# Performance work log

Measured on AMD Instinct MI355X. Metric: run time of the kernel, lower is better.

Reference implementation:

```python
import jax, jax.numpy as jnp
import numpy as np

B, S, D, F, E, K = 4, 2048, 1024, 4096, 8, 2


def setup_inputs() -> dict:
    key = jax.random.key(0)
    ks = jax.random.split(key, 8)
    x = jax.random.normal(ks[0], (B, S, D), dtype=jnp.float32)
    # torch nn.Linear stores W as (out, in); stack per-expert params on leading E axis
    router_w = jax.random.normal(ks[1], (E, D), dtype=jnp.float32) * 0.02
    w1_w = jax.random.normal(ks[2], (E, F, D), dtype=jnp.float32) * 0.02
    w1_b = jax.random.normal(ks[3], (E, F), dtype=jnp.float32) * 0.02
    w2_w = jax.random.normal(ks[4], (E, D, F), dtype=jnp.float32) * 0.02
    w2_b = jax.random.normal(ks[5], (E, D), dtype=jnp.float32) * 0.02
    wg_w = jax.random.normal(ks[6], (E, F, D), dtype=jnp.float32) * 0.02
    wg_b = jax.random.normal(ks[7], (E, F), dtype=jnp.float32) * 0.02
    return {"x": x, "router_w": router_w, "w1_w": w1_w, "w1_b": w1_b,
            "w2_w": w2_w, "w2_b": w2_b, "wg_w": wg_w, "wg_b": wg_b}


def reference(x, router_w, w1_w, w1_b, w2_w, w2_b, wg_w, wg_b):
    # router: softmax then top-k (identical to torch.topk(softmax(...)))
    probs = jax.nn.softmax(jnp.einsum('bsd,ed->bse', x, router_w), axis=-1)
    token_probs, probs_idx = jax.lax.top_k(probs, K)  # (b,s,k)
    # combine the k gate weights into a dense (b,s,E) gate (top-k indices are distinct,
    # so summing one-hot slots reproduces the original scatter + sum over k exactly)
    gates = jnp.sum(token_probs[..., None] *
                    jax.nn.one_hot(probs_idx, E, dtype=x.dtype), axis=-2)  # (b,s,E)
    gates_e = jnp.moveaxis(gates, -1, 0)  # (E,b,s)

    def body(acc, params):
        w1w, w1b, w2w, w2b, wgw, wgb, g = params
        y = jax.nn.gelu(jnp.einsum('bsd,fd->bsf', x, wgw) + wgb, approximate=False)
        h = y * (jnp.einsum('bsd,fd->bsf', x, w1w) + w1b)
        out = jnp.einsum('bsf,df->bsd', h, w2w) + w2b
        return acc + out * g[..., None], None

    acc0 = jnp.zeros_like(x)
    out, _ = jax.lax.scan(body, acc0, (w1_w, w1_b, w2_w, w2_b, wg_w, wg_b, gates_e))
    return out
```

## Files before the change

kernel.cpp:

```cpp
#include <hip/hip_runtime.h>
#include <hip/hip_bf16.h>

#define TOK 8192
#define DD 1024
#define FF 4096
#define EE 8
#define NPAIR 16384

typedef __attribute__((ext_vector_type(8))) short short8;
typedef __attribute__((ext_vector_type(4))) short short4v;
typedef __attribute__((ext_vector_type(4))) float f32x4;

#define VMCNT8()  asm volatile("s_waitcnt vmcnt(8)" ::: "memory")
#define VMCNT0()  asm volatile("s_waitcnt vmcnt(0)" ::: "memory")
#define LGKM0()   asm volatile("s_waitcnt lgkmcnt(0)" ::: "memory")
#define BARRIER() asm volatile("s_barrier" ::: "memory")

__device__ __forceinline__ void async16(const void* g, void* l) {
  __builtin_amdgcn_global_load_lds((const __attribute__((address_space(1))) void*)g,
                                   (__attribute__((address_space(3))) void*)l, 16, 0, 0);
}

__device__ __forceinline__ short bfc(float f) {
  return __builtin_bit_cast(short, (__bf16)f);
}
__device__ __forceinline__ short8 cvt8(f32x4 a, f32x4 b) {
  short8 r;
  r[0]=bfc(a[0]); r[1]=bfc(a[1]); r[2]=bfc(a[2]); r[3]=bfc(a[3]);
  r[4]=bfc(b[0]); r[5]=bfc(b[1]); r[6]=bfc(b[2]); r[7]=bfc(b[3]);
  return r;
}
__device__ __forceinline__ int swz4(int r) { return (r ^ (r >> 2)) & 3; }

__global__ __launch_bounds__(256) void cvt_bf16_kernel(const float* __restrict__ src,
                                                       short* __restrict__ dst, int n8) {
  int i = blockIdx.x * 256 + threadIdx.x;
  const int stride = gridDim.x * 256;
  for (; i < n8; i += stride) {
    f32x4 a = ((const f32x4*)src)[2*i];
    f32x4 b = ((const f32x4*)src)[2*i + 1];
    ((short8*)dst)[i] = cvt8(a, b);
  }
}

__global__ __launch_bounds__(256) void cvt_interleave(const float* __restrict__ wgw,
    const float* __restrict__ w1w, short* __restrict__ wB) {
  const int b = blockIdx.x;
  const int e = b >> 12;
  const int f = b & 4095;
  const int g = f >> 4, j = f & 15;
  const int tid = threadIdx.x;
  const int u = tid & 127;
  const float* src = ((tid < 128) ? wgw : w1w) + (size_t)b * DD;
  const size_t drow = (size_t)e * (2*FF) + 32*g + j + ((tid < 128) ? 0 : 16);
  f32x4 a = ((const f32x4*)src)[2*u];
  f32x4 c = ((const f32x4*)src)[2*u + 1];
  ((short8*)(wB + drow * DD))[u] = cvt8(a, c);
}

__global__ __launch_bounds__(64) void router_kernel(const float* __restrict__ x,
    const float* __restrict__ rw, int* __restrict__ counts, int* __restrict__ lists,
    float* __restrict__ gates, int* __restrict__ eids, short* __restrict__ xb, int write_xb) {
  const int t = blockIdx.x;
  const int l = threadIdx.x;
  const f32x4* xr = (const f32x4*)(x + (size_t)t * DD);
  f32x4 xv[4];
#pragma unroll
  for (int i = 0; i < 4; i++) xv[i] = xr[l + 64 * i];
  if (write_xb) {
    short4v* xo = (short4v*)(xb + (size_t)t * DD);
#pragma unroll
    for (int i = 0; i < 4; i++) {
      short4v o; o[0]=bfc(xv[i][0]); o[1]=bfc(xv[i][1]); o[2]=bfc(xv[i][2]); o[3]=bfc(xv[i][3]);
      xo[l + 64 * i] = o;
    }
  }
  float lg[EE];
#pragma unroll
  for (int e = 0; e < EE; e++) {
    const f32x4* wr = (const f32x4*)(rw + e * DD);
    float s = 0.f;
#pragma unroll
    for (int i = 0; i < 4; i++) {
      f32x4 w = wr[l + 64 * i];
      s += xv[i][0]*w[0] + xv[i][1]*w[1] + xv[i][2]*w[2] + xv[i][3]*w[3];
    }
#pragma unroll
    for (int off = 32; off > 0; off >>= 1) s += __shfl_down(s, off, 64);
    lg[e] = s;
  }
  if (l == 0) {
    float mx = lg[0];
#pragma unroll
    for (int e = 1; e < EE; e++) mx = fmaxf(mx, lg[e]);
    float p[EE]; float den = 0.f;
#pragma unroll
    for (int e = 0; e < EE; e++) { p[e] = expf(lg[e] - mx); den += p[e]; }
    int i1 = 0;
#pragma unroll
    for (int e = 1; e < EE; e++) if (p[e] > p[i1]) i1 = e;
    int i2 = (i1 == 0) ? 1 : 0;
#pragma unroll
    for (int e = 0; e < EE; e++) if (e != i1 && p[e] > p[i2]) i2 = e;
    float inv = 1.f / den;
    gates[t*2+0] = p[i1] * inv;  eids[t*2+0] = i1;
    gates[t*2+1] = p[i2] * inv;  eids[t*2+1] = i2;
    int p1 = atomicAdd(&counts[i1], 1); lists[i1*TOK + p1] = t*2 + 0;
    int p2 = atomicAdd(&counts[i2], 1); lists[i2*TOK + p2] = t*2 + 1;
  }
}

#define TBUF 16384

#define STGA(buf, t) do { const int ko=(t)*32; short* dd=&ldsm[(buf)*TBUF]; \
    async16(aS1+ko, dd + wid*512); async16(aS2+ko, dd + 4096 + wid*512); } while(0)
#define STGB(buf, t) do { const int ko=(t)*32; short* dd=&ldsm[(buf)*TBUF + 8192]; \
    async16(bS1+ko, dd + wid*512); async16(bS2+ko, dd + 4096 + wid*512); } while(0)
#define RDA(buf, mi) (*(const short8*)&ldsm[(buf)*TBUF + (wr*128+(mi)*16+ln15)*32 + ((g ^ swz4(wr*128+(mi)*16+ln15))*8)])
#define RDB(buf, ni) (*(const short8*)&ldsm[(buf)*TBUF + 8192 + (wc*64+(ni)*16+ln15)*32 + ((g ^ swz4(wc*64+(ni)*16+ln15))*8)])

#define MFMA_BF16 __builtin_amdgcn_mfma_f32_16x16x32_bf16

#define KLOOP(NT)                                                              \
  STGA(0,0); STGB(0,0); STGA(1,1); STGB(1,1); STGA(2,2); STGB(2,2);            \
  VMCNT8(); BARRIER();                                                         \
  _Pragma("unroll 1")                                                          \
  for (int t = 0; t < (NT); t++) {                                             \
    const int cur = t & 3, pf = (t + 3) & 3;                                   \
    const int tp = (t + 3 < (NT)) ? t + 3 : 0;       \
    short8 a[8], b[4];                                                         \
    _Pragma("unroll")                                                          \
    for (int mi = 0; mi < 8; mi++) a[mi] = RDA(cur, mi);                       \
    _Pragma("unroll")                                                          \
    for (int ni = 0; ni < 4; ni++) b[ni] = RDB(cur, ni);                       \
    STGA(pf, tp); STGB(pf, tp);                                                \
    VMCNT8();                                                                  \
    LGKM0();                                                                   \
    BARRIER();                                                                 \
    __builtin_amdgcn_s_setprio(1);                                             \
    _Pragma("unroll")                                                          \
    for (int mi = 0; mi < 8; mi++) {                                           \
      _Pragma("unroll")                                                        \
      for (int ni = 0; ni < 4; ni++)                                           \
        acc[mi][ni] = MFMA_BF16(a[mi], b[ni], acc[mi][ni], 0, 0, 0);           \
    }                                                                          \
    __builtin_amdgcn_s_setprio(0);                                             \
  }                                                                            \
  VMCNT0();

__global__ __launch_bounds__(512, 1) void stage_a8(
    const short* __restrict__ xb, const short* __restrict__ wB,
    const float* __restrict__ wgb, const float* __restrict__ w1b,
    const int* __restrict__ counts, const int* __restrict__ lists,
    short* __restrict__ hbuf, int f0chunk, int Fc) {

  const int NBX = gridDim.x, NBY = gridDim.y;
  const int q = NBX * NBY;
  const int lin = blockIdx.x + NBX * (blockIdx.y + NBY * blockIdx.z);
  const int orig = (lin & 7) * q + (lin >> 3);
  const int e = orig / q;
  const int m = orig - e * q;
  const int by = m % NBY;
  const int bx = m / NBY;

  const int cnt = counts[e];
  const int row0 = bx * 256;
  if (row0 >= cnt) return;
  const int R0 = f0chunk * 2 + by * 256;

  __shared__ short ldsm[4 * TBUF];
  __shared__ int s_pair[256];

  const int tid = threadIdx.x;
  const int wid = tid >> 6;
  const int lane = tid & 63;
  const int ln15 = lane & 15, g = lane >> 4;
  const int wr = wid >> 2, wc = wid & 3;

  if (tid < 256) {
    int r = row0 + tid;
    s_pair[tid] = (r < cnt) ? lists[e*TOK + r] : 0;
  }
  __syncthreads();

  const int r1 = tid >> 2, s1 = tid & 3;
  const int r2 = r1 + 128;
  const int l1 = s1 ^ swz4(r1);
  const int l2 = s1 ^ swz4(r2);
  const short* aS1 = xb + (size_t)(s_pair[r1] >> 1) * DD + l1 * 8;
  const short* aS2 = xb + (size_t)(s_pair[r2] >> 1) * DD + l2 * 8;
  const short* bS1 = wB + ((size_t)e * (2*FF) + R0 + r1) * DD + l1 * 8;
  const short* bS2 = wB + ((size_t)e * (2*FF) + R0 + r2) * DD + l2 * 8;

  f32x4 acc[8][4] = {};

  KLOOP(32)

  const float* wgb_e = wgb + e * FF;
  const float* w1b_e = w1b + e * FF;
  float bgv[2], b1v[2]; int fl[2];
#pragma unroll
  for (int m2 = 0; m2 < 2; m2++) {
    int fg = (R0 + wc*64 + m2*32) / 2 + ln15;
    bgv[m2] = wgb_e[fg];
    b1v[m2] = w1b_e[fg];
    fl[m2] = fg - f0chunk;
  }
#pragma unroll
  for (int mi = 0; mi < 8; mi++) {
    int trb = wr*128 + mi*16 + (g << 2);
#pragma unroll
    for (int m2 = 0; m2 < 2; m2++) {
#pragma unroll
      for (int j = 0; j < 4; j++) {
        int tr = trb + j;
        if (row0 + tr < cnt) {
          int pair = s_pair[tr];
          float hg = acc[mi][2*m2][j] + bgv[m2];
          float h1 = acc[mi][2*m2+1][j] + b1v[m2];
          float gl = 0.5f * hg * (1.f + erff(hg * 0.70710678118f));
          hbuf[(size_t)pair * Fc + fl[m2]] = bfc(gl * h1);
        }
      }
    }
  }
}

__global__ __launch_bounds__(512, 1) void stage_b8(
    const short* __restrict__ hbuf, const short* __restrict__ w2wb,
    const int* __restrict__ counts, const int* __restrict__ lists,
    float* __restrict__ ybuf, int Fc) {

  const int NBX = gridDim.x, NBY = gridDim.y;
  const int q = NBX * NBY;
  const int lin = blockIdx.x + NBX * (blockIdx.y + NBY * blockIdx.z);
  const int orig = (lin & 7) * q + (lin >> 3);
  const int e = orig / q;
  const int m = orig - e * q;
  const int by = m % NBY;
  const int bx = m / NBY;

  const int cnt = counts[e];
  const int row0 = bx * 256;
  if (row0 >= cnt) return;
  const int d0 = by * 256;

  __shared__ short ldsm[4 * TBUF];
  __shared__ int s_pair[256];

  const int tid = threadIdx.x;
  const int wid = tid >> 6;
  const int lane = tid & 63;
  const int ln15 = lane & 15, g = lane >> 4;
  const int wr = wid >> 2, wc = wid & 3;

  if (tid < 256) {
    int r = row0 + tid;
    s_pair[tid] = (r < cnt) ? lists[e*TOK + r] : 0;
  }
  __syncthreads();

  const int r1 = tid >> 2, s1 = tid & 3;
  const int r2 = r1 + 128;
  const int l1 = s1 ^ swz4(r1);
  const int l2 = s1 ^ swz4(r2);
  const short* aS1 = hbuf + (size_t)s_pair[r1] * Fc + l1 * 8;
  const short* aS2 = hbuf + (size_t)s_pair[r2] * Fc + l2 * 8;
  const short* bS1 = w2wb + ((size_t)e * DD + d0 + r1) * FF + l1 * 8;
  const short* bS2 = w2wb + ((size_t)e * DD + d0 + r2) * FF + l2 * 8;

  f32x4 acc[8][4] = {};
  const int NT = Fc >> 5;

  KLOOP(NT)

#pragma unroll
  for (int mi = 0; mi < 8; mi++) {
    int trb = wr*128 + mi*16 + (g << 2);
#pragma unroll
    for (int j = 0; j < 4; j++) {
      int tr = trb + j;
      if (row0 + tr < cnt) {
        int pair = s_pair[tr];
        float* yrow = ybuf + (size_t)pair * DD;
#pragma unroll
        for (int ni = 0; ni < 4; ni++) {
          int d = d0 + wc*64 + ni*16 + ln15;
          yrow[d] = acc[mi][ni][j];
        }
      }
    }
  }
}

__global__ __launch_bounds__(256) void combine_kernel(const float* __restrict__ yb,
    const float* __restrict__ w2b, const float* __restrict__ gates,
    const int* __restrict__ eids, float* __restrict__ out) {
  const int t = blockIdx.x;
  const int tid = threadIdx.x;
  const float g0 = gates[2*t], g1 = gates[2*t+1];
  const int e0 = eids[2*t], e1 = eids[2*t+1];
  f32x4 y0 = ((const f32x4*)(yb + (size_t)(2*t) * DD))[tid];
  f32x4 y1 = ((const f32x4*)(yb + (size_t)(2*t+1) * DD))[tid];
  f32x4 c0 = ((const f32x4*)(w2b + (size_t)e0 * DD))[tid];
  f32x4 c1 = ((const f32x4*)(w2b + (size_t)e1 * DD))[tid];
  f32x4 o;
#pragma unroll
  for (int i = 0; i < 4; i++) o[i] = g0 * (y0[i] + c0[i]) + g1 * (y1[i] + c1[i]);
  ((f32x4*)(out + (size_t)t * DD))[tid] = o;
}

#define BB_LDS (128*64)
__global__ __launch_bounds__(256, 2) void stage_b_bf(
    const short* __restrict__ hbuf, const short* __restrict__ w2wb, const float* __restrict__ w2b,
    const int* __restrict__ counts, const int* __restrict__ lists, const float* __restrict__ gates,
    float* __restrict__ out, int f0chunk, int Fc, int addbias) {

  const int lin = blockIdx.x + 64 * (blockIdx.y + 8 * blockIdx.z);
  const int orig = (lin & 7) * 512 + (lin >> 3);
  const int bx = orig & 63;
  const int by = (orig >> 6) & 7;
  const int e  = orig >> 9;

  const int cnt = counts[e];
  const int row0 = bx * 128;
  if (row0 >= cnt) return;
  const int d0 = by * 128;

  __shared__ short lA[2 * BB_LDS];
  __shared__ short lB[2 * BB_LDS];
  __shared__ int s_pair[128];

  const int tid = threadIdx.x;
  const int wid = tid >> 6;
  const int lane = tid & 63;

  if (tid < 128) {
    int r = row0 + tid;
    s_pair[tid] = (r < cnt) ? lists[e*TOK + r] : 0;
  }
  __syncthreads();

  const short* aSrc[4]; const short* bSrc[4];
#pragma unroll
  for (int p = 0; p < 4; p++) {
    int j = p * 256 + tid;
    int r = j >> 3;
    int sl = (j & 7) ^ (r & 7);
    aSrc[p] = hbuf + (size_t)s_pair[r] * Fc + sl * 8;
    bSrc[p] = w2wb + ((size_t)e * DD + d0 + r) * FF + f0chunk + sl * 8;
  }

  f32x4 acc[4][4] = {};
  const int wr = wid >> 1, wc = wid & 1;
  const int NT = Fc >> 6;

#pragma unroll
  for (int p = 0; p < 4; p++) async16(aSrc[p], &lA[p*2048 + wid*512]);
#pragma unroll
  for (int p = 0; p < 4; p++) async16(bSrc[p], &lB[p*2048 + wid*512]);

  for (int t = 0; t < NT; t++) {
    const int cur = t & 1;
    if (t + 1 < NT) {
      const int nb = cur ^ 1;
      const int kf = (t + 1) * 64;
#pragma unroll
      for (int p = 0; p < 4; p++) async16(aSrc[p] + kf, &lA[nb*BB_LDS + p*2048 + wid*512]);
#pragma unroll
      for (int p = 0; p < 4; p++) async16(bSrc[p] + kf, &lB[nb*BB_LDS + p*2048 + wid*512]);
      VMCNT8();
    } else {
      VMCNT0();
    }
    BARRIER();

    const short* LA = lA + cur * BB_LDS;
    const short* LB = lB + cur * BB_LDS;
#pragma unroll
    for (int kk = 0; kk < 2; kk++) {
      short8 a[4], b[4];
#pragma unroll
      for (int mi = 0; mi < 4; mi++) {
        int r = wr*64 + mi*16 + (lane & 15);
        int u = (kk*4 + (lane >> 4)) ^ (r & 7);
        a[mi] = *(const short8*)(LA + r*64 + u*8);
      }
#pragma unroll
      for (int ni = 0; ni < 4; ni++) {
        int r = wc*64 + ni*16 + (lane & 15);
        int u = (kk*4 + (lane >> 4)) ^ (r & 7);
        b[ni] = *(const short8*)(LB + r*64 + u*8);
      }
#pragma unroll
      for (int mi = 0; mi < 4; mi++)
#pragma unroll
        for (int ni = 0; ni < 4; ni++)
          acc[mi][ni] = MFMA_BF16(a[mi], b[ni], acc[mi][ni], 0, 0, 0);
    }
    BARRIER();
  }

  const float* w2b_e = w2b + e * DD;
#pragma unroll
  for (int mi = 0; mi < 4; mi++) {
    int trb = wr*64 + mi*16 + ((lane >> 4) << 2);
#pragma unroll
    for (int j = 0; j < 4; j++) {
      int tr = trb + j;
      if (row0 + tr < cnt) {
        int pair = s_pair[tr];
        int t = pair >> 1;
        float gt = gates[pair];
        float* orow = out + (size_t)t * DD;
#pragma unroll
        for (int ni = 0; ni < 4; ni++) {
          int d = d0 + wc*64 + ni*16 + (lane & 15);
          float v = acc[mi][ni][j] * gt;
          if (addbias) v += w2b_e[d] * gt;
          atomicAdd(orow + d, v);
        }
      }
    }
  }
}

__global__ __launch_bounds__(256, 2) void stage_a_f32(
    const float* __restrict__ x, const float* __restrict__ wgw, const float* __restrict__ wgb,
    const float* __restrict__ w1w, const float* __restrict__ w1b,
    const int* __restrict__ counts, const int* __restrict__ lists,
    short* __restrict__ hbuf, int f0chunk, int Fc) {

  const int e = blockIdx.z;
  const int cnt = counts[e];
  const int row0 = blockIdx.x * 128;
  if (row0 >= cnt) return;
  const int fc0 = blockIdx.y * 128;
  const int fg0 = f0chunk + fc0;

  __shared__ float lA[128 * 32];
  __shared__ float lBg[128 * 32];
  __shared__ float lB1[128 * 32];
  __shared__ int s_pair[128];

  const int tid = threadIdx.x;
  const int wid = tid >> 6;
  const int lane = tid & 63;

  if (tid < 128) {
    int r = row0 + tid;
    s_pair[tid] = (r < cnt) ? lists[e*TOK + r] : 0;
  }
  __syncthreads();

  const float* aSrc[4]; const float* gSrc[4]; const float* oSrc[4];
#pragma unroll
  for (int p = 0; p < 4; p++) {
    int j = p * 256 + tid;
    int r = j >> 3;
    int sl = (j & 7) ^ (r & 7);
    aSrc[p] = x + (size_t)(s_pair[r] >> 1) * DD + sl * 4;
    gSrc[p] = wgw + ((size_t)e * FF + fg0 + r) * DD + sl * 4;
    oSrc[p] = w1w + ((size_t)e * FF + fg0 + r) * DD + sl * 4;
  }

  f32x4 accg[4][4] = {}; f32x4 acc1[4][4] = {};
  const int wr = wid >> 1, wc = wid & 1;

  for (int k0 = 0; k0 < DD; k0 += 32) {
#pragma unroll
    for (int p = 0; p < 4; p++) async16(aSrc[p] + k0, &lA[p*1024 + wid*256]);
#pragma unroll
    for (int p = 0; p < 4; p++) async16(gSrc[p] + k0, &lBg[p*1024 + wid*256]);
#pragma unroll
    for (int p = 0; p < 4; p++) async16(oSrc[p] + k0, &lB1[p*1024 + wid*256]);
    __syncthreads();

    short8 a[4], bg[4], b1[4];
#pragma unroll
    for (int mi = 0; mi < 4; mi++) {
      int r = wr*64 + mi*16 + (lane & 15);
      int g2 = (lane >> 4) * 2;
      const f32x4* Ar = (const f32x4*)&lA[r * 32];
      a[mi] = cvt8(Ar[g2 ^ (r & 7)], Ar[(g2 + 1) ^ (r & 7)]);
    }
#pragma unroll
    for (int ni = 0; ni < 4; ni++) {
      int r = wc*64 + ni*16 + (lane & 15);
      int g2 = (lane >> 4) * 2;
      const f32x4* Bg = (const f32x4*)&lBg[r * 32];
      const f32x4* B1 = (const f32x4*)&lB1[r * 32];
      bg[ni] = cvt8(Bg[g2 ^ (r & 7)], Bg[(g2 + 1) ^ (r & 7)]);
      b1[ni] = cvt8(B1[g2 ^ (r & 7)], B1[(g2 + 1) ^ (r & 7)]);
    }
#pragma unroll
    for (int mi = 0; mi < 4; mi++)
#pragma unroll
      for (int ni = 0; ni < 4; ni++) {
        accg[mi][ni] = MFMA_BF16(a[mi], bg[ni], accg[mi][ni], 0, 0, 0);
        acc1[mi][ni] = MFMA_BF16(a[mi], b1[ni], acc1[mi][ni], 0, 0, 0);
      }
    __syncthreads();
  }

  const float* wgb_e = wgb + e * FF;
  const float* w1b_e = w1b + e * FF;
#pragma unroll
  for (int mi = 0; mi < 4; mi++) {
    int trb = wr*64 + mi*16 + ((lane >> 4) << 2);
#pragma unroll
    for (int ni = 0; ni < 4; ni++) {
      int c = wc*64 + ni*16 + (lane & 15);
      float bgv = wgb_e[fg0 + c];
      float b1v = w1b_e[fg0 + c];
#pragma unroll
      for (int j = 0; j < 4; j++) {
        int tr = trb + j;
        if (row0 + tr < cnt) {
          int pair = s_pair[tr];
          float hg = accg[mi][ni][j] + bgv;
          float h1 = acc1[mi][ni][j] + b1v;
          float gl = 0.5f * hg * (1.f + erff(hg * 0.70710678118f));
          hbuf[(size_t)pair * Fc + fc0 + c] = bfc(gl * h1);
        }
      }
    }
  }
}

__global__ __launch_bounds__(256, 2) void stage_b_f32(
    const short* __restrict__ hbuf, const float* __restrict__ w2w, const float* __restrict__ w2b,
    const int* __restrict__ counts, const int* __restrict__ lists, const float* __restrict__ gates,
    float* __restrict__ out, int f0chunk, int Fc, int addbias) {

  const int e = blockIdx.z;
  const int cnt = counts[e];
  const int row0 = blockIdx.x * 128;
  if (row0 >= cnt) return;
  const int d0 = blockIdx.y * 128;

  __shared__ short lA[128 * 64];
  __shared__ float lB[128 * 64];
  __shared__ int s_pair[128];

  const int tid = threadIdx.x;
  const int wid = tid >> 6;
  const int lane = tid & 63;

  if (tid < 128) {
    int r = row0 + tid;
    s_pair[tid] = (r < cnt) ? lists[e*TOK + r] : 0;
  }
  __syncthreads();

  const short* aSrc[4];
#pragma unroll
  for (int p = 0; p < 4; p++) {
    int j = p * 256 + tid;
    int r = j >> 3;
    int sl = (j & 7) ^ (r & 7);
    aSrc[p] = hbuf + (size_t)s_pair[r] * Fc + sl * 8;
  }
  const float* bSrc[8];
#pragma unroll
  for (int p = 0; p < 8; p++) {
    int j = p * 256 + tid;
    int r = j >> 4;
    int sl = (j & 15) ^ (r & 7);
    bSrc[p] = w2w + ((size_t)e * DD + d0 + r) * FF + f0chunk + sl * 4;
  }

  f32x4 acc[4][4] = {};
  const int wr = wid >> 1, wc = wid & 1;

  for (int kf = 0; kf < Fc; kf += 64) {
#pragma unroll
    for (int p = 0; p < 4; p++) async16(aSrc[p] + kf, &lA[p*2048 + wid*512]);
#pragma unroll
    for (int p = 0; p < 8; p++) async16(bSrc[p] + kf, &lB[p*1024 + wid*256]);
    __syncthreads();

#pragma unroll
    for (int kk = 0; kk < 2; kk++) {
      short8 a[4]; short8 b[4];
#pragma unroll
      for (int mi = 0; mi < 4; mi++) {
        int r = wr*64 + mi*16 + (lane & 15);
        int u = (kk*4 + (lane >> 4)) ^ (r & 7);
        a[mi] = ((const short8*)(lA + r * 64))[u];
      }
#pragma unroll
      for (int ni = 0; ni < 4; ni++) {
        int r = wc*64 + ni*16 + (lane & 15);
        int g2 = (kk*4 + (lane >> 4)) * 2;
        const f32x4* Br = (const f32x4*)(lB + r * 64);
        b[ni] = cvt8(Br[g2 ^ (r & 7)], Br[(g2 + 1) ^ (r & 7)]);
      }
#pragma unroll
      for (int mi = 0; mi < 4; mi++)
#pragma unroll
        for (int ni = 0; ni < 4; ni++)
          acc[mi][ni] = MFMA_BF16(a[mi], b[ni], acc[mi][ni], 0, 0, 0);
    }
    __syncthreads();
  }

  const float* w2b_e = w2b + e * DD;
#pragma unroll
  for (int mi = 0; mi < 4; mi++) {
    int trb = wr*64 + mi*16 + ((lane >> 4) << 2);
#pragma unroll
    for (int j = 0; j < 4; j++) {
      int tr = trb + j;
      if (row0 + tr < cnt) {
        int pair = s_pair[tr];
        int t = pair >> 1;
        float gt = gates[pair];
        float* orow = out + (size_t)t * DD;
#pragma unroll
        for (int ni = 0; ni < 4; ni++) {
          int d = d0 + wc*64 + ni*16 + (lane & 15);
          float v = acc[mi][ni][j] * gt;
          if (addbias) v += w2b_e[d] * gt;
          atomicAdd(orow + d, v);
        }
      }
    }
  }
}

extern "C" void kernel_launch(void* const* d_in, const int* in_sizes, int n_in,
                              void* d_out, int out_size, void* d_ws, size_t ws_size,
                              hipStream_t stream) {
  const float* x   = (const float*)d_in[0];
  const float* rw  = (const float*)d_in[1];
  const float* w1w = (const float*)d_in[2];
  const float* w1b = (const float*)d_in[3];
  const float* w2w = (const float*)d_in[4];
  const float* w2b = (const float*)d_in[5];
  const float* wgw = (const float*)d_in[6];
  const float* wgb = (const float*)d_in[7];
  float* out = (float*)d_out;

  char* ws = (char*)d_ws;
  size_t off = 0;
  int* counts = (int*)(ws + off); off += 128;
  int* lists  = (int*)(ws + off); off += (size_t)EE * TOK * 4;
  float* gates = (float*)(ws + off); off += (size_t)NPAIR * 4;
  int* eids = (int*)(ws + off); off += (size_t)NPAIR * 4;
  const size_t base0 = off;

  const size_t WELEM = (size_t)EE * FF * DD;
  const size_t bf_need = base0 + (size_t)TOK*DD*2 + 2*WELEM*2 + WELEM*2;

  hipMemsetAsync(counts, 0, 128, stream);

  const int cands[6] = {4096, 2048, 1024, 512, 256, 128};

  if (bf_need + (size_t)NPAIR * 128 * 2 <= ws_size) {
    off = base0;
    short* xb   = (short*)(ws + off); off += (size_t)TOK * DD * 2;
    short* wB   = (short*)(ws + off); off += 2 * WELEM * 2;
    short* w2wb = (short*)(ws + off); off += WELEM * 2;
    short* hbuf = (short*)(ws + off);
    float* ybuf = (float*)wB;

    int Fc = 128;
    for (int i = 0; i < 6; i++)
      if (off + (size_t)NPAIR * cands[i] * 2 <= ws_size) { Fc = cands[i]; break; }

    router_kernel<<<dim3(TOK), dim3(64), 0, stream>>>(x, rw, counts, lists, gates, eids, xb, 1);
    cvt_interleave<<<dim3(EE*FF), dim3(256), 0, stream>>>(wgw, w1w, wB);
    cvt_bf16_kernel<<<dim3(2048), dim3(256), 0, stream>>>(w2w, w2wb, (int)(WELEM/8));

    if (Fc == 4096) {
      stage_a8<<<dim3(32, (2*Fc)/256, EE), dim3(512), 0, stream>>>(
          xb, wB, wgb, w1b, counts, lists, hbuf, 0, Fc);
      stage_b8<<<dim3(32, DD/256, EE), dim3(512), 0, stream>>>(
          hbuf, w2wb, counts, lists, ybuf, Fc);
      combine_kernel<<<dim3(TOK), dim3(256), 0, stream>>>(ybuf, w2b, gates, eids, out);
    } else {
      hipMemsetAsync(out, 0, (size_t)TOK * DD * 4, stream);
      for (int f0 = 0; f0 < FF; f0 += Fc) {
        stage_a8<<<dim3(32, (2*Fc)/256, EE), dim3(512), 0, stream>>>(
            xb, wB, wgb, w1b, counts, lists, hbuf, f0, Fc);
        stage_b_bf<<<dim3(64, DD/128, EE), dim3(256), 0, stream>>>(
            hbuf, w2wb, w2b, counts, lists, gates, out, f0, Fc, f0 == 0);
      }
    }
  } else {
    short* hbuf = (short*)(ws + base0);
    int Fc = 128;
    for (int i = 0; i < 6; i++)
      if (base0 + (size_t)NPAIR * cands[i] * 2 <= ws_size) { Fc = cands[i]; break; }

    hipMemsetAsync(out, 0, (size_t)TOK * DD * 4, stream);
    router_kernel<<<dim3(TOK), dim3(64), 0, stream>>>(x, rw, counts, lists, gates, eids, nullptr, 0);

    for (int f0 = 0; f0 < FF; f0 += Fc) {
      dim3 ga(64, Fc / 128, EE);
      stage_a_f32<<<ga, dim3(256), 0, stream>>>(x, wgw, wgb, w1w, w1b, counts, lists, hbuf, f0, Fc);
      dim3 gb(64, DD / 128, EE);
      stage_b_f32<<<gb, dim3(256), 0, stream>>>(hbuf, w2w, w2b, counts, lists, gates, out, f0, Fc, f0 == 0);
    }
  }
}
```

Baseline: 1.009 ms.

## Double-buffer MFMA operand registers so LDS reads overlap the previous tile's MFMAs

```diff
diff --git a/kernel.cpp b/kernel.cpp
--- a/kernel.cpp
+++ b/kernel.cpp
@@ -15,6 +15,7 @@
 #define VMCNT0()  asm volatile("s_waitcnt vmcnt(0)" ::: "memory")
 #define LGKM0()   asm volatile("s_waitcnt lgkmcnt(0)" ::: "memory")
 #define BARRIER() asm volatile("s_barrier" ::: "memory")
+#define SCHEDB()  __builtin_amdgcn_sched_barrier(0)
 
 __device__ __forceinline__ void async16(const void* g, void* l) {
   __builtin_amdgcn_global_load_lds((const __attribute__((address_space(1))) void*)g,
@@ -121,30 +122,54 @@
 
 #define MFMA_BF16 __builtin_amdgcn_mfma_f32_16x16x32_bf16
 
-#define KLOOP(NT)                                                              \
-  STGA(0,0); STGB(0,0); STGA(1,1); STGB(1,1); STGA(2,2); STGB(2,2);            \
-  VMCNT8(); BARRIER();                                                         \
-  _Pragma("unroll 1")                                                          \
-  for (int t = 0; t < (NT); t++) {                                             \
-    const int cur = t & 3, pf = (t + 3) & 3;                                   \
-    const int tp = (t + 3 < (NT)) ? t + 3 : 0;       \
-    short8 a[8], b[4];                                                         \
-    _Pragma("unroll")                                                          \
-    for (int mi = 0; mi < 8; mi++) a[mi] = RDA(cur, mi);                       \
-    _Pragma("unroll")                                                          \
-    for (int ni = 0; ni < 4; ni++) b[ni] = RDB(cur, ni);                       \
+#define KBODY(tt, RC, RN, NT)                                                  \
+  {                                                                            \
+    const int pf = ((tt) + 3) & 3;                                             \
+    const int tp = ((tt) + 3 < (NT)) ? (tt) + 3 : 0;   \
     STGA(pf, tp); STGB(pf, tp);                                                \
+    SCHEDB();                                                                  \
     VMCNT8();                                                                  \
+    SCHEDB();                                                                  \
     LGKM0();                                                                   \
-    BARRIER();                                                                 \
+    SCHEDB();                                                                  \
+    __builtin_amdgcn_s_barrier();                                              \
+    SCHEDB();                                                                  \
+    if ((tt) + 1 < (NT)) {                                                     \
+      const int nb = ((tt) + 1) & 3;                                           \
+      _Pragma("unroll")                                                        \
+      for (int mi = 0; mi < 8; mi++) RN##a[mi] = RDA(nb, mi);                  \
+      _Pragma("unroll")                                                        \
+      for (int ni = 0; ni < 4; ni++) RN##b[ni] = RDB(nb, ni);                  \
+    }                                                                          \
+    SCHEDB();                                                                  \
     __builtin_amdgcn_s_setprio(1);                                             \
     _Pragma("unroll")                                                          \
-    for (int mi = 0; mi < 8; mi++) {                                           \
+    for (int mi = 0; mi < 8; mi++)                                             \
       _Pragma("unroll")                                                        \
       for (int ni = 0; ni < 4; ni++)                                           \
-        acc[mi][ni] = MFMA_BF16(a[mi], b[ni], acc[mi][ni], 0, 0, 0);           \
-    }                                                                          \
+        acc[mi][ni] = MFMA_BF16(RC##a[mi], RC##b[ni], acc[mi][ni], 0, 0, 0);   \
     __builtin_amdgcn_s_setprio(0);                                             \
+    SCHEDB();                                                                  \
+  }
+
+#define KLOOP2(NT)                                                             \
+  short8 Pa[8], Pb[4], Qa[8], Qb[4];                                           \
+  STGA(0,0); STGB(0,0); STGA(1,1); STGB(1,1); STGA(2,2); STGB(2,2);            \
+  SCHEDB();                                                                    \
+  VMCNT8();                                                                    \
+  SCHEDB();                                                                    \
+  __builtin_amdgcn_s_barrier();                                                \
+  SCHEDB();                                                                    \
+  _Pragma("unroll")                                                            \
+  for (int mi = 0; mi < 8; mi++) Pa[mi] = RDA(0, mi);                          \
+  _Pragma("unroll")                                                            \
+  for (int ni = 0; ni < 4; ni++) Pb[ni] = RDB(0, ni);                          \
+  SCHEDB();                                                                    \
+  _Pragma("unroll 1")                                                          \
+  for (int t2 = 0; t2 < (NT)/2; t2++) {                                        \
+    const int t0 = 2*t2;                                                       \
+    KBODY(t0,     P, Q, NT);                                                   \
+    KBODY(t0 + 1, Q, P, NT);                                                   \
   }                                                                            \
   VMCNT0();
 
@@ -194,7 +219,7 @@
 
   f32x4 acc[8][4] = {};
 
-  KLOOP(32)
+  KLOOP2(32)
 
   const float* wgb_e = wgb + e * FF;
   const float* w1b_e = w1b + e * FF;
@@ -272,7 +297,7 @@
   f32x4 acc[8][4] = {};
   const int NT = Fc >> 5;
 
-  KLOOP(NT)
+  KLOOP2(NT)
 
 #pragma unroll
   for (int mi = 0; mi < 8; mi++) {
```

Result: slower. 1.062 ms (+5.2%).

## Switch GEMM K-loop to double-buffered 64-wide K tiles with 8-way swizzle

Applied to the files above, without the earlier changes.

```diff
diff --git a/kernel.cpp b/kernel.cpp
--- a/kernel.cpp
+++ b/kernel.cpp
@@ -15,6 +15,7 @@
 #define VMCNT0()  asm volatile("s_waitcnt vmcnt(0)" ::: "memory")
 #define LGKM0()   asm volatile("s_waitcnt lgkmcnt(0)" ::: "memory")
 #define BARRIER() asm volatile("s_barrier" ::: "memory")
+#define SCHEDB()  __builtin_amdgcn_sched_barrier(0)
 
 __device__ __forceinline__ void async16(const void* g, void* l) {
   __builtin_amdgcn_global_load_lds((const __attribute__((address_space(1))) void*)g,
@@ -30,7 +31,6 @@
   r[4]=bfc(b[0]); r[5]=bfc(b[1]); r[6]=bfc(b[2]); r[7]=bfc(b[3]);
   return r;
 }
-__device__ __forceinline__ int swz4(int r) { return (r ^ (r >> 2)) & 3; }
 
 __global__ __launch_bounds__(256) void cvt_bf16_kernel(const float* __restrict__ src,
                                                        short* __restrict__ dst, int n8) {
@@ -110,41 +110,56 @@
   }
 }
 
-#define TBUF 16384
-
-#define STGA(buf, t) do { const int ko=(t)*32; short* dd=&ldsm[(buf)*TBUF]; \
-    async16(aS1+ko, dd + wid*512); async16(aS2+ko, dd + 4096 + wid*512); } while(0)
-#define STGB(buf, t) do { const int ko=(t)*32; short* dd=&ldsm[(buf)*TBUF + 8192]; \
-    async16(bS1+ko, dd + wid*512); async16(bS2+ko, dd + 4096 + wid*512); } while(0)
-#define RDA(buf, mi) (*(const short8*)&ldsm[(buf)*TBUF + (wr*128+(mi)*16+ln15)*32 + ((g ^ swz4(wr*128+(mi)*16+ln15))*8)])
-#define RDB(buf, ni) (*(const short8*)&ldsm[(buf)*TBUF + 8192 + (wc*64+(ni)*16+ln15)*32 + ((g ^ swz4(wc*64+(ni)*16+ln15))*8)])
+#define TB2 32768
+
+#define STG2(buf, t) do { const int ko=(t)*64;                                 \
+    _Pragma("unroll")                                                          \
+    for (int p = 0; p < 4; p++) {                                              \
+      async16(aS[p] + ko, &ldsm[(buf)*TB2 + p*4096 + wid*512]);                \
+      async16(bS[p] + ko, &ldsm[(buf)*TB2 + 16384 + p*4096 + wid*512]);        \
+    } } while(0)
+
+#define RD_A(buf, kk, mi) (*(const short8*)&ldsm[(buf)*TB2 + (wr*128+(mi)*16+ln15)*64 + ((((kk)*4+g) ^ ((wr*128+(mi)*16+ln15)&7))*8)])
+#define RD_B(buf, kk, ni) (*(const short8*)&ldsm[(buf)*TB2 + 16384 + (wc*64+(ni)*16+ln15)*64 + ((((kk)*4+g) ^ ((wc*64+(ni)*16+ln15)&7))*8)])
 
 #define MFMA_BF16 __builtin_amdgcn_mfma_f32_16x16x32_bf16
 
-#define KLOOP(NT)                                                              \
-  STGA(0,0); STGB(0,0); STGA(1,1); STGB(1,1); STGA(2,2); STGB(2,2);            \
-  VMCNT8(); BARRIER();                                                         \
+#define KLOOP3(NT)                                                             \
+  STG2(0, 0);                                                                  \
+  SCHEDB();                                                                    \
   _Pragma("unroll 1")                                                          \
   for (int t = 0; t < (NT); t++) {                                             \
-    const int cur = t & 3, pf = (t + 3) & 3;                                   \
-    const int tp = (t + 3 < (NT)) ? t + 3 : 0;       \
-    short8 a[8], b[4];                                                         \
+    const int cur = t & 1;                                                     \
+    if (t + 1 < (NT)) {                                                        \
+      STG2(cur ^ 1, t + 1);                                                    \
+      SCHEDB();                                                                \
+      VMCNT8();                                                                \
+    } else {                                                                   \
+      VMCNT0();                                                                \
+    }                                                                          \
+    SCHEDB();                                                                  \
+    __builtin_amdgcn_s_barrier();                                              \
+    SCHEDB();                                                                  \
     _Pragma("unroll")                                                          \
-    for (int mi = 0; mi < 8; mi++) a[mi] = RDA(cur, mi);                       \
-    _Pragma("unroll")                                                          \
-    for (int ni = 0; ni < 4; ni++) b[ni] = RDB(cur, ni);                       \
-    STGA(pf, tp); STGB(pf, tp);                                                \
-    VMCNT8();                                                                  \
+    for (int kk = 0; kk < 2; kk++) {                                           \
+      short8 a[8], b[4];                                                       \
+      _Pragma("unroll")                                                        \
+      for (int mi = 0; mi < 8; mi++) a[mi] = RD_A(cur, kk, mi);                \
+      _Pragma("unroll")                                                        \
+      for (int ni = 0; ni < 4; ni++) b[ni] = RD_B(cur, kk, ni);                \
+      __builtin_amdgcn_s_setprio(1);                                           \
+      _Pragma("unroll")                                                        \
+      for (int mi = 0; mi < 8; mi++)                                           \
+        _Pragma("unroll")                                                      \
+        for (int ni = 0; ni < 4; ni++)                                         \
+          acc[mi][ni] = MFMA_BF16(a[mi], b[ni], acc[mi][ni], 0, 0, 0);         \
+      __builtin_amdgcn_s_setprio(0);                                           \
+    }                                                                          \
+    SCHEDB();                                                                  \
     LGKM0();                                                                   \
-    BARRIER();                                                                 \
-    __builtin_amdgcn_s_setprio(1);                                             \
-    _Pragma("unroll")                                                          \
-    for (int mi = 0; mi < 8; mi++) {                                           \
-      _Pragma("unroll")                                                        \
-      for (int ni = 0; ni < 4; ni++)                                           \
-        acc[mi][ni] = MFMA_BF16(a[mi], b[ni], acc[mi][ni], 0, 0, 0);           \
-    }                                                                          \
-    __builtin_amdgcn_s_setprio(0);                                             \
+    SCHEDB();                                                                  \
+    __builtin_amdgcn_s_barrier();                                              \
+    SCHEDB();                                                                  \
   }                                                                            \
   VMCNT0();
 
@@ -168,7 +183,7 @@
   if (row0 >= cnt) return;
   const int R0 = f0chunk * 2 + by * 256;
 
-  __shared__ short ldsm[4 * TBUF];
+  __shared__ short ldsm[2 * TB2];
   __shared__ int s_pair[256];
 
   const int tid = threadIdx.x;
@@ -183,18 +198,19 @@
   }
   __syncthreads();
 
-  const int r1 = tid >> 2, s1 = tid & 3;
-  const int r2 = r1 + 128;
-  const int l1 = s1 ^ swz4(r1);
-  const int l2 = s1 ^ swz4(r2);
-  const short* aS1 = xb + (size_t)(s_pair[r1] >> 1) * DD + l1 * 8;
-  const short* aS2 = xb + (size_t)(s_pair[r2] >> 1) * DD + l2 * 8;
-  const short* bS1 = wB + ((size_t)e * (2*FF) + R0 + r1) * DD + l1 * 8;
-  const short* bS2 = wB + ((size_t)e * (2*FF) + R0 + r2) * DD + l2 * 8;
+  const short* aS[4]; const short* bS[4];
+#pragma unroll
+  for (int p = 0; p < 4; p++) {
+    int j = p * 512 + tid;
+    int r = j >> 3;
+    int sl = (j & 7) ^ (r & 7);
+    aS[p] = xb + (size_t)(s_pair[r] >> 1) * DD + sl * 8;
+    bS[p] = wB + ((size_t)e * (2*FF) + R0 + r) * DD + sl * 8;
+  }
 
   f32x4 acc[8][4] = {};
 
-  KLOOP(32)
+  KLOOP3(16)
 
   const float* wgb_e = wgb + e * FF;
   const float* w1b_e = w1b + e * FF;
@@ -245,7 +261,7 @@
   if (row0 >= cnt) return;
   const int d0 = by * 256;
 
-  __shared__ short ldsm[4 * TBUF];
+  __shared__ short ldsm[2 * TB2];
   __shared__ int s_pair[256];
 
   const int tid = threadIdx.x;
@@ -260,19 +276,20 @@
   }
   __syncthreads();
 
-  const int r1 = tid >> 2, s1 = tid & 3;
-  const int r2 = r1 + 128;
-  const int l1 = s1 ^ swz4(r1);
-  const int l2 = s1 ^ swz4(r2);
-  const short* aS1 = hbuf + (size_t)s_pair[r1] * Fc + l1 * 8;
-  const short* aS2 = hbuf + (size_t)s_pair[r2] * Fc + l2 * 8;
-  const short* bS1 = w2wb + ((size_t)e * DD + d0 + r1) * FF + l1 * 8;
-  const short* bS2 = w2wb + ((size_t)e * DD + d0 + r2) * FF + l2 * 8;
+  const short* aS[4]; const short* bS[4];
+#pragma unroll
+  for (int p = 0; p < 4; p++) {
+    int j = p * 512 + tid;
+    int r = j >> 3;
+    int sl = (j & 7) ^ (r & 7);
+    aS[p] = hbuf + (size_t)s_pair[r] * Fc + sl * 8;
+    bS[p] = w2wb + ((size_t)e * DD + d0 + r) * FF + sl * 8;
+  }
 
   f32x4 acc[8][4] = {};
-  const int NT = Fc >> 5;
-
-  KLOOP(NT)
+  const int NT = Fc >> 6;
+
+  KLOOP3(NT)
 
 #pragma unroll
   for (int mi = 0; mi < 8; mi++) {
```

Result: slower. 1.053 ms (+4.4%).
